# Kernel tuning notes

Hardware: AMD Instinct MI355X
Metric: run time of the kernel (lower is better)

## Reference

```python
import jax, jax.numpy as jnp
import numpy as np


def _conv_same(x, k):
    # x: [C, H, W] single sample; k: [C_out, C_in, 3, 3] per-sample kernel
    return jax.lax.conv_general_dilated(
        x[None], k, window_strides=(1, 1), padding='SAME',
        dimension_numbers=('NCHW', 'OIHW', 'NCHW'))[0]


_batched_conv = jax.vmap(_conv_same)  # maps over batch of inputs and batch of kernels


def setup_inputs() -> dict:
    key = jax.random.key(0)
    k1, k2, k3 = jax.random.split(key, 3)
    B, C, H, W = 16, 256, 64, 64
    x = jax.random.normal(k1, (B, C, H, W), dtype=jnp.float32)
    # scale kernels down so pre-relu activations stay in a sane range
    kernel1 = jax.random.normal(k2, (B, C, C, 3, 3), dtype=jnp.float32) * 0.02
    kernel2 = jax.random.normal(k3, (B, C, C, 3, 3), dtype=jnp.float32) * 0.02
    return {"x": x, "kernel1": kernel1, "kernel2": kernel2}


def reference(x, kernel1, kernel2):
    # per-sample conv1 -> relu -> per-sample conv2 -> residual add -> relu
    h = jax.nn.relu(_batched_conv(x, kernel1))          # [B, C, H, W]
    out = jax.nn.relu(x + _batched_conv(h, kernel2))    # [B, C, H, W]
    return out
```

## Files before the change

kernel.cpp:

```cpp
#include <hip/hip_runtime.h>
#include <hip/hip_bf16.h>
#include <stdint.h>

typedef __attribute__((ext_vector_type(8))) short bf16x8;
typedef __attribute__((ext_vector_type(4))) float f32x4;
typedef __attribute__((address_space(1))) const void g_void;
typedef __attribute__((address_space(3))) void l_void;

#define NB 16
#define NC 256
#define NHW 4096
#define NT 72
#define SLOTB 32768

__global__ __launch_bounds__(256) void prep_xt2(const float* __restrict__ x,
                                                __hip_bfloat16* __restrict__ xt2,
                                                float* __restrict__ zp) {
  __shared__ float tile[64][65];
  const int b = blockIdx.z;
  const int cb = blockIdx.y << 6;
  const int pb = blockIdx.x << 6;
  if (blockIdx.x == 0 && blockIdx.y == 0 && blockIdx.z == 0) {
#pragma unroll
    for (int q = 0; q < 8; ++q) zp[(q << 8) + threadIdx.x] = 0.f;
  }
  const float* xs = x + ((size_t)(b * NC + cb) << 12) + pb;
#pragma unroll
  for (int k = 0; k < 16; ++k) {
    int idx = threadIdx.x + (k << 8);
    int c = idx >> 6, p = idx & 63;
    tile[p][c] = xs[((size_t)c << 12) + p];
  }
  __syncthreads();
#pragma unroll
  for (int k = 0; k < 16; ++k) {
    int idx = threadIdx.x + (k << 8);
    int p = idx >> 6, c = idx & 63;
    int P = pb + p, C = cb + c;
    xt2[((size_t)(b * 8 + (C >> 5)) << 17) + ((size_t)P << 5) + (C & 31)] =
        __float2bfloat16(tile[p][c]);
  }
}

__global__ __launch_bounds__(256) void prep_kt2(const float* __restrict__ kin,
                                                __hip_bfloat16* __restrict__ kt2) {
  const int bco = blockIdx.x;
  const int b = bco >> 8, co = bco & 255;
  const size_t base = (size_t)bco * 2304;
  const int ci = threadIdx.x;
  float v[9];
#pragma unroll
  for (int s = 0; s < 9; ++s) v[s] = kin[base + ci * 9 + s];
  const int cib = ci >> 5, chunk = (ci >> 3) & 3, e = ci & 7;
  const int sc = chunk ^ ((co >> 1) & 3);
#pragma unroll
  for (int s = 0; s < 9; ++s) {
    const size_t dst = (((size_t)(b * NT + cib * 9 + s)) << 13) +
                       (co << 5) + (sc << 3) + e;
    kt2[dst] = __float2bfloat16(v[s]);
  }
}

template <int PASS>
__global__ __launch_bounds__(512, 2) void conv_gemm(
    const __hip_bfloat16* __restrict__ img2,
    const __hip_bfloat16* __restrict__ kt2,
    const float* __restrict__ xres,
    const __hip_bfloat16* __restrict__ zp,
    void* __restrict__ outp) {
  __shared__ __align__(16) char L[4 * SLOTB];

  const int tid = threadIdx.x;
  const int lane = tid & 63;
  const int wid = tid >> 6;
  const int wm = wid >> 2;
  const int wn = wid & 3;

  const int orig = blockIdx.x;
  const int g = ((orig & 7) << 5) + (orig >> 3);
  const int b = g >> 4;
  const int ptile = g & 15;
  const int pbase = ptile << 8;

  const char* xb = (const char*)img2 + ((size_t)b << 21);
  const char* ktb = (const char*)kt2 + ((size_t)(b * NT) << 14);
  const char* zpb = (const char*)zp;

  const int srow = lane >> 2;
  const int sch = (lane & 3) ^ ((srow >> 1) & 3);

  int aoff[8], boff[4];
#pragma unroll
  for (int i = 0; i < 8; ++i) {
    const int ma = (wm << 7) + (i << 4) + (lane & 15);
    aoff[i] = (ma << 6) + ((((lane >> 4) ^ ((ma >> 1) & 3))) << 4);
  }
#pragma unroll
  for (int j = 0; j < 4; ++j) {
    const int nb = (wn << 6) + (j << 4) + (lane & 15);
    boff[j] = (nb << 6) + ((((lane >> 4) ^ ((nb >> 1) & 3))) << 4);
  }
  const bool killlo = (lane & 15) == 0;
  const bool killhi = (lane & 15) == 15;
  const bf16x8 z8 = {0, 0, 0, 0, 0, 0, 0, 0};

  f32x4 acc[8][4];
#pragma unroll
  for (int i = 0; i < 8; ++i)
#pragma unroll
    for (int j = 0; j < 4; ++j) acc[i][j] = (f32x4){0.f, 0.f, 0.f, 0.f};

  auto stageI = [&](int tn, int cibp, int dh, int dw, bool dummy) {
    char* dst0 = L + (tn & 3) * SLOTB;
    const char* cb = xb + ((size_t)(cibp & 7) << 18);
#pragma unroll
    for (int i = 0; i < 2; ++i) {
      const int grp = (i << 3) + wid;
      const int h = (ptile << 2) + (grp >> 2) + dh;
      const bool ok = !dummy && ((unsigned)h < 64u);
      const int off = ((pbase + (grp << 4) + srow + (dh << 6) + dw) << 6) + (sch << 4);
      const char* src = ok ? cb + off : zpb + (lane << 4);
      __builtin_amdgcn_global_load_lds((g_void*)src, (l_void*)(dst0 + (grp << 10)), 16, 0, 0);
    }
  };
  auto stageKer = [&](int tn, bool dummy) {
    char* dst0 = L + (tn & 3) * SLOTB + 16384;
    const char* src0 = ktb + ((size_t)tn << 14);
#pragma unroll
    for (int i = 0; i < 2; ++i) {
      const int grp = (i << 3) + wid;
      const char* src = !dummy ? src0 + (grp << 10) + (lane << 4) : zpb + (lane << 4);
      __builtin_amdgcn_global_load_lds((g_void*)src, (l_void*)(dst0 + (grp << 10)), 16, 0, 0);
    }
  };
  auto stageM = [&](int tn, int cibp, int dh, int dw, bool dummy) {
    if (PASS == 1) stageI(tn, cibp, dh, dw, dummy); else stageKer(tn, dummy);
  };
  auto stageN = [&](int tn, int cibp, int dh, int dw, bool dummy) {
    if (PASS == 1) stageKer(tn, dummy); else stageI(tn, cibp, dh, dw, dummy);
  };

  stageN(0, 0, -1, -1, false);
  stageM(0, 0, -1, -1, false);
  stageN(1, 0, -1, 0, false);
  stageM(1, 0, -1, 0, false);
  stageN(2, 0, -1, 1, false);
  stageM(2, 0, -1, 1, false);
  stageN(3, 0, 0, -1, false);
  asm volatile("s_waitcnt vmcnt(10)" ::: "memory");
  __builtin_amdgcn_s_barrier();
  __builtin_amdgcn_sched_barrier(0);

#pragma unroll 1
  for (int c8 = 0; c8 < 8; ++c8) {
#pragma unroll
    for (int s = 0; s < 9; ++s) {
      const int kk = c8 * 9 + s;
      const int sl = (c8 + s) & 3;
      const char* At = L + sl * SLOTB + ((PASS == 1) ? 0 : 16384);
      const char* Bt = L + sl * SLOTB + ((PASS == 1) ? 16384 : 0);
      const int dw = s % 3 - 1;

      bf16x8 fal[4], fb[4];
#pragma unroll
      for (int i = 0; i < 4; ++i) fal[i] = *(const bf16x8*)(At + aoff[i]);
#pragma unroll
      for (int j = 0; j < 4; ++j) fb[j] = *(const bf16x8*)(Bt + boff[j]);
      {
        const int s3 = (s + 3) % 9;
        stageM(kk + 3, c8 + (s + 3) / 9, s3 / 3 - 1, s3 % 3 - 1, kk + 3 >= NT);
      }
      __builtin_amdgcn_s_barrier();
      asm volatile("s_waitcnt lgkmcnt(0)" ::: "memory");
      __builtin_amdgcn_sched_barrier(0);
      if (PASS == 1) {
        if (dw == -1) fal[0] = killlo ? z8 : fal[0];
        if (dw == 1) fal[3] = killhi ? z8 : fal[3];
      } else {
        if (dw == -1) fb[0] = killlo ? z8 : fb[0];
        if (dw == 1) fb[3] = killhi ? z8 : fb[3];
      }
      __builtin_amdgcn_s_setprio(1);
#pragma unroll
      for (int i = 0; i < 4; ++i)
#pragma unroll
        for (int j = 0; j < 4; ++j)
          acc[i][j] = __builtin_amdgcn_mfma_f32_16x16x32_bf16(fal[i], fb[j], acc[i][j], 0, 0, 0);
      __builtin_amdgcn_s_setprio(0);
      __builtin_amdgcn_s_barrier();
      __builtin_amdgcn_sched_barrier(0);

      bf16x8 fah[4];
#pragma unroll
      for (int i = 0; i < 4; ++i) fah[i] = *(const bf16x8*)(At + aoff[4 + i]);
      {
        const int s4 = (s + 4) % 9;
        stageN(kk + 4, c8 + (s + 4) / 9, s4 / 3 - 1, s4 % 3 - 1, kk + 4 >= NT);
      }
      __builtin_amdgcn_s_barrier();
      asm volatile("s_waitcnt lgkmcnt(0)" ::: "memory");
      __builtin_amdgcn_sched_barrier(0);
      if (PASS == 1) {
        if (dw == -1) fah[0] = killlo ? z8 : fah[0];
        if (dw == 1) fah[3] = killhi ? z8 : fah[3];
      }
      __builtin_amdgcn_s_setprio(1);
#pragma unroll
      for (int i = 0; i < 4; ++i)
#pragma unroll
        for (int j = 0; j < 4; ++j)
          acc[4 + i][j] =
              __builtin_amdgcn_mfma_f32_16x16x32_bf16(fah[i], fb[j], acc[4 + i][j], 0, 0, 0);
      __builtin_amdgcn_s_setprio(0);
      asm volatile("s_waitcnt vmcnt(6)" ::: "memory");
      __builtin_amdgcn_s_barrier();
      __builtin_amdgcn_sched_barrier(0);
    }
  }
  asm volatile("s_waitcnt vmcnt(0)" ::: "memory");
  __builtin_amdgcn_sched_barrier(0);

  const int lg = lane >> 4;
  const int ln = lane & 15;
  if (PASS == 1) {
    __hip_bfloat16* ho = (__hip_bfloat16*)outp;
#pragma unroll
    for (int i = 0; i < 8; ++i)
#pragma unroll
      for (int j = 0; j < 4; ++j)
#pragma unroll
        for (int r = 0; r < 4; ++r) {
          int pixel = pbase + (wm << 7) + (i << 4) + (lg << 2) + r;
          int co = (wn << 6) + (j << 4) + ln;
          float v = acc[i][j][r];
          v = v > 0.f ? v : 0.f;
          ho[((size_t)(b * 8 + (co >> 5)) << 17) + ((size_t)pixel << 5) + (co & 31)] =
              __float2bfloat16(v);
        }
  } else {
    float* oo = (float*)outp;
#pragma unroll
    for (int i = 0; i < 8; ++i)
#pragma unroll
      for (int j = 0; j < 4; ++j)
#pragma unroll
        for (int r = 0; r < 4; ++r) {
          int co = (wm << 7) + (i << 4) + (lg << 2) + r;
          int pixel = pbase + (wn << 6) + (j << 4) + ln;
          size_t idx = ((size_t)(b * NC + co) << 12) + pixel;
          float v = acc[i][j][r] + xres[idx];
          oo[idx] = v > 0.f ? v : 0.f;
        }
  }
}

extern "C" void kernel_launch(void* const* d_in, const int* in_sizes, int n_in,
                              void* d_out, int out_size, void* d_ws, size_t ws_size,
                              hipStream_t stream) {
  const float* x = (const float*)d_in[0];
  const float* k1 = (const float*)d_in[1];
  const float* k2 = (const float*)d_in[2];

  char* w = (char*)d_ws;
  __hip_bfloat16* xt2 = (__hip_bfloat16*)(w + 256);
  __hip_bfloat16* ht2 = xt2 + (size_t)NB * 8 * NHW * 32;
  __hip_bfloat16* kt2 = ht2 + (size_t)NB * 8 * NHW * 32;
  float* zp = (float*)(kt2 + (size_t)NB * NT * 256 * 32);

  prep_xt2<<<dim3(64, 4, NB), 256, 0, stream>>>(x, xt2, zp);
  prep_kt2<<<dim3(NB * NC), 256, 0, stream>>>(k1, kt2);
  conv_gemm<1><<<dim3(256), 512, 0, stream>>>(xt2, kt2, nullptr,
                                              (const __hip_bfloat16*)zp, (void*)ht2);
  prep_kt2<<<dim3(NB * NC), 256, 0, stream>>>(k2, kt2);
  conv_gemm<2><<<dim3(256), 512, 0, stream>>>(ht2, kt2, x,
                                              (const __hip_bfloat16*)zp, d_out);
}
```

Baseline: 186.0 us.

## Restructure conv GEMM to three-slot LDS pipeline with one phase per step

The four-slot LDS ring, where A and B tiles were staged at staggered half-step offsets, becomes a three-slot ring. Both operands of tile kk+2 are staged together, and each K-step now runs as one phase: load all 8 A fragments and 4 B fragments, then issue 32 MFMAs. This halves the barriers and lgkmcnt waits per step and cuts LDS use from 128KB to 96KB. In exchange, prefetch depth drops from about 3.5 tiles to 2, so global load latency has less room to hide, and more fragment registers are live at once.

Result: no change. 183.4 us (-1.4%).

```diff
diff --git a/kernel.cpp b/kernel.cpp
--- a/kernel.cpp
+++ b/kernel.cpp
@@ -68,7 +68,7 @@
     const float* __restrict__ xres,
     const __hip_bfloat16* __restrict__ zp,
     void* __restrict__ outp) {
-  __shared__ __align__(16) char L[4 * SLOTB];
+  __shared__ __align__(16) char L[3 * SLOTB];
 
   const int tid = threadIdx.x;
   const int lane = tid & 63;
@@ -111,7 +111,7 @@
     for (int j = 0; j < 4; ++j) acc[i][j] = (f32x4){0.f, 0.f, 0.f, 0.f};
 
   auto stageI = [&](int tn, int cibp, int dh, int dw, bool dummy) {
-    char* dst0 = L + (tn & 3) * SLOTB;
+    char* dst0 = L + (tn % 3) * SLOTB;
     const char* cb = xb + ((size_t)(cibp & 7) << 18);
 #pragma unroll
     for (int i = 0; i < 2; ++i) {
@@ -124,7 +124,7 @@
     }
   };
   auto stageKer = [&](int tn, bool dummy) {
-    char* dst0 = L + (tn & 3) * SLOTB + 16384;
+    char* dst0 = L + (tn % 3) * SLOTB + 16384;
     const char* src0 = ktb + ((size_t)tn << 14);
 #pragma unroll
     for (int i = 0; i < 2; ++i) {
@@ -133,86 +133,60 @@
       __builtin_amdgcn_global_load_lds((g_void*)src, (l_void*)(dst0 + (grp << 10)), 16, 0, 0);
     }
   };
-  auto stageM = [&](int tn, int cibp, int dh, int dw, bool dummy) {
-    if (PASS == 1) stageI(tn, cibp, dh, dw, dummy); else stageKer(tn, dummy);
+  auto stageBoth = [&](int tn, int cibp, int dh, int dw, bool dummy) {
+    stageI(tn, cibp, dh, dw, dummy);
+    stageKer(tn, dummy);
   };
-  auto stageN = [&](int tn, int cibp, int dh, int dw, bool dummy) {
-    if (PASS == 1) stageKer(tn, dummy); else stageI(tn, cibp, dh, dw, dummy);
-  };
-
-  stageN(0, 0, -1, -1, false);
-  stageM(0, 0, -1, -1, false);
-  stageN(1, 0, -1, 0, false);
-  stageM(1, 0, -1, 0, false);
-  stageN(2, 0, -1, 1, false);
-  stageM(2, 0, -1, 1, false);
-  stageN(3, 0, 0, -1, false);
-  asm volatile("s_waitcnt vmcnt(10)" ::: "memory");
+
+  stageBoth(0, 0, -1, -1, false);
+  stageBoth(1, 0, -1, 0, false);
+  asm volatile("s_waitcnt vmcnt(4)" ::: "memory");
   __builtin_amdgcn_s_barrier();
   __builtin_amdgcn_sched_barrier(0);
 
 #pragma unroll 1
-  for (int c8 = 0; c8 < 8; ++c8) {
+  for (int c9 = 0; c9 < 8; ++c9) {
 #pragma unroll
     for (int s = 0; s < 9; ++s) {
-      const int kk = c8 * 9 + s;
-      const int sl = (c8 + s) & 3;
+      const int kk = c9 * 9 + s;
+      const int sl = s % 3;
       const char* At = L + sl * SLOTB + ((PASS == 1) ? 0 : 16384);
       const char* Bt = L + sl * SLOTB + ((PASS == 1) ? 16384 : 0);
       const int dw = s % 3 - 1;
 
-      bf16x8 fal[4], fb[4];
-#pragma unroll
-      for (int i = 0; i < 4; ++i) fal[i] = *(const bf16x8*)(At + aoff[i]);
+      bf16x8 fa[8], fb[4];
+#pragma unroll
+      for (int i = 0; i < 8; ++i) fa[i] = *(const bf16x8*)(At + aoff[i]);
 #pragma unroll
       for (int j = 0; j < 4; ++j) fb[j] = *(const bf16x8*)(Bt + boff[j]);
       {
-        const int s3 = (s + 3) % 9;
-        stageM(kk + 3, c8 + (s + 3) / 9, s3 / 3 - 1, s3 % 3 - 1, kk + 3 >= NT);
+        const int s2 = (s + 2) % 9;
+        stageBoth(kk + 2, c9 + (s + 2) / 9, s2 / 3 - 1, s2 % 3 - 1, kk + 2 >= NT);
       }
       __builtin_amdgcn_s_barrier();
       asm volatile("s_waitcnt lgkmcnt(0)" ::: "memory");
       __builtin_amdgcn_sched_barrier(0);
       if (PASS == 1) {
-        if (dw == -1) fal[0] = killlo ? z8 : fal[0];
-        if (dw == 1) fal[3] = killhi ? z8 : fal[3];
+        if (dw == -1) {
+          fa[0] = killlo ? z8 : fa[0];
+          fa[4] = killlo ? z8 : fa[4];
+        }
+        if (dw == 1) {
+          fa[3] = killhi ? z8 : fa[3];
+          fa[7] = killhi ? z8 : fa[7];
+        }
       } else {
         if (dw == -1) fb[0] = killlo ? z8 : fb[0];
         if (dw == 1) fb[3] = killhi ? z8 : fb[3];
       }
       __builtin_amdgcn_s_setprio(1);
 #pragma unroll
-      for (int i = 0; i < 4; ++i)
+      for (int i = 0; i < 8; ++i)
 #pragma unroll
         for (int j = 0; j < 4; ++j)
-          acc[i][j] = __builtin_amdgcn_mfma_f32_16x16x32_bf16(fal[i], fb[j], acc[i][j], 0, 0, 0);
+          acc[i][j] = __builtin_amdgcn_mfma_f32_16x16x32_bf16(fa[i], fb[j], acc[i][j], 0, 0, 0);
       __builtin_amdgcn_s_setprio(0);
-      __builtin_amdgcn_s_barrier();
-      __builtin_amdgcn_sched_barrier(0);
-
-      bf16x8 fah[4];
-#pragma unroll
-      for (int i = 0; i < 4; ++i) fah[i] = *(const bf16x8*)(At + aoff[4 + i]);
-      {
-        const int s4 = (s + 4) % 9;
-        stageN(kk + 4, c8 + (s + 4) / 9, s4 / 3 - 1, s4 % 3 - 1, kk + 4 >= NT);
-      }
-      __builtin_amdgcn_s_barrier();
-      asm volatile("s_waitcnt lgkmcnt(0)" ::: "memory");
-      __builtin_amdgcn_sched_barrier(0);
-      if (PASS == 1) {
-        if (dw == -1) fah[0] = killlo ? z8 : fah[0];
-        if (dw == 1) fah[3] = killhi ? z8 : fah[3];
-      }
-      __builtin_amdgcn_s_setprio(1);
-#pragma unroll
-      for (int i = 0; i < 4; ++i)
-#pragma unroll
-        for (int j = 0; j < 4; ++j)
-          acc[4 + i][j] =
-              __builtin_amdgcn_mfma_f32_16x16x32_bf16(fah[i], fb[j], acc[4 + i][j], 0, 0, 0);
-      __builtin_amdgcn_s_setprio(0);
-      asm volatile("s_waitcnt vmcnt(6)" ::: "memory");
+      asm volatile("s_waitcnt vmcnt(4)" ::: "memory");
       __builtin_amdgcn_s_barrier();
       __builtin_amdgcn_sched_barrier(0);
     }
```
